# Performance work log

Hardware: AMD Instinct MI355X
Metric: run time of the kernel (lower is better)

## Reference

```python
import jax, jax.numpy as jnp
import numpy as np

TEMPERATURE = 8.0  # sqrt(d_k=64)
NEG_INF = -1.0e9   # matches masked_fill value in source


def setup_inputs() -> dict:
    key = jax.random.key(0)
    kq, kk, kv, km = jax.random.split(key, 4)
    B, H, T, C = 2, 16, 2048, 64
    q = jax.random.normal(kq, (B, H, T, C), dtype=jnp.float32)
    k = jax.random.normal(kk, (B, H, T, C), dtype=jnp.float32)
    v = jax.random.normal(kv, (B, H, T, C), dtype=jnp.float32)
    mask = jax.random.randint(km, (B, 1, T, T), 0, 2, dtype=jnp.int32)
    return {"q": q, "k": k, "v": v, "mask": mask}


def reference(q, k, v, mask):
    # attn = (q / temperature) @ k^T   -> [b, h, T, T]
    attn = jnp.einsum("bhqc,bhkc->bhqk", q / TEMPERATURE, k)
    attn = jnp.where(mask == 0, NEG_INF, attn)
    attn = jax.nn.softmax(attn, axis=-1)
    # dropout is identity in eval / deterministic reference
    output = jnp.einsum("bhqk,bhkc->bhqc", attn, v)
    return (output, attn)
```

## Files before the change

### kernel.cpp

```cpp
#include <hip/hip_runtime.h>
#include <stdint.h>
#include <stddef.h>

#define T_DIM 2048
#define C_DIM 64
#define SCALE_L2E 0.18033688011112042f
#define STG_P 40

typedef __bf16 bf16x8 __attribute__((ext_vector_type(8)));
typedef float f32x4 __attribute__((ext_vector_type(4)));
typedef unsigned int u32x4 __attribute__((ext_vector_type(4)));
typedef unsigned int u32x2 __attribute__((ext_vector_type(2)));
typedef int i32x4 __attribute__((ext_vector_type(4)));
typedef unsigned short u16t;

static __device__ __forceinline__ unsigned f2bf_bits(float f) {
  unsigned u = __builtin_bit_cast(unsigned, f);
  u += 0x7fffu + ((u >> 16) & 1u);
  return u >> 16;
}
static __device__ __forceinline__ bf16x8 asfrag(u32x4 u) {
  return __builtin_bit_cast(bf16x8, u);
}
static __device__ __forceinline__ bf16x8 pack8(f32x4 a, f32x4 b) {
  u32x4 u;
  u[0] = f2bf_bits(a[0]) | (f2bf_bits(a[1]) << 16);
  u[1] = f2bf_bits(a[2]) | (f2bf_bits(a[3]) << 16);
  u[2] = f2bf_bits(b[0]) | (f2bf_bits(b[1]) << 16);
  u[3] = f2bf_bits(b[2]) | (f2bf_bits(b[3]) << 16);
  return __builtin_bit_cast(bf16x8, u);
}
static __device__ __forceinline__ bf16x8 ld_cvt8(const float* p) {
  return pack8(*(const f32x4*)p, *(const f32x4*)(p + 4));
}
static __device__ __forceinline__ float bf_lo(unsigned u) {
  return __builtin_bit_cast(float, u << 16);
}
static __device__ __forceinline__ float bf_hi(unsigned u) {
  return __builtin_bit_cast(float, u & 0xffff0000u);
}

__global__ __launch_bounds__(256) void prep_kernel(
    const float* __restrict__ k, const float* __restrict__ v,
    const int* __restrict__ mask, u16t* __restrict__ kb,
    u16t* __restrict__ vt2, unsigned* __restrict__ mb) {
  if (blockIdx.x < 2048) {
    const size_t e0 = ((size_t)blockIdx.x * 256 + threadIdx.x) * 8;
    const float* src = k + e0;
    u32x4 u;
    f32x4 a = *(const f32x4*)src;
    f32x4 b = *(const f32x4*)(src + 4);
    u[0] = f2bf_bits(a[0]) | (f2bf_bits(a[1]) << 16);
    u[1] = f2bf_bits(a[2]) | (f2bf_bits(a[3]) << 16);
    u[2] = f2bf_bits(b[0]) | (f2bf_bits(b[1]) << 16);
    u[3] = f2bf_bits(b[2]) | (f2bf_bits(b[3]) << 16);
    *(u32x4*)(kb + e0) = u;
  } else if (blockIdx.x < 4096) {
    __shared__ float tile[32][66];
    const int t = threadIdx.x;
    const int tl = blockIdx.x - 2048;
    const int bh = tl >> 6;
    const int t32 = tl & 63;
    const float* src = v + ((size_t)bh * T_DIM + t32 * 32) * C_DIM;
#pragma unroll
    for (int u = 0; u < 2; ++u) {
      const int vec = t + u * 256;
      const int jj = vec >> 4;
      const int c4 = (vec & 15) * 4;
      const f32x4 x = *(const f32x4*)(src + jj * C_DIM + c4);
      tile[jj][c4] = x[0];
      tile[jj][c4 + 1] = x[1];
      tile[jj][c4 + 2] = x[2];
      tile[jj][c4 + 3] = x[3];
    }
    __syncthreads();
    const int c = t >> 2;
    const int j8 = (t & 3) * 8;
    u32x4 o;
#pragma unroll
    for (int i = 0; i < 4; ++i) {
      o[i] = f2bf_bits(tile[j8 + 2 * i][c]) |
             (f2bf_bits(tile[j8 + 2 * i + 1][c]) << 16);
    }
    *(u32x4*)(vt2 + ((size_t)bh * 64 + t32) * 2048 + (size_t)t * 8) = o;
  } else {
    const int gid = (blockIdx.x - 4096) * 256 + threadIdx.x;
    const int* src = mask + (size_t)gid * 32;
    unsigned bits = 0;
#pragma unroll
    for (int t = 0; t < 8; ++t) {
      i32x4 x = *(const i32x4*)(src + t * 4);
      bits |= (x[0] != 0 ? 1u : 0u) << (t * 4);
      bits |= (x[1] != 0 ? 1u : 0u) << (t * 4 + 1);
      bits |= (x[2] != 0 ? 1u : 0u) << (t * 4 + 2);
      bits |= (x[3] != 0 ? 1u : 0u) << (t * 4 + 3);
    }
    mb[gid] = bits;
  }
}

template <bool USE_PREP>
__global__ __launch_bounds__(256, 3) void attn_fwd(
    const float* __restrict__ qp, const float* __restrict__ kp,
    const float* __restrict__ vp, const int* __restrict__ maskp,
    const u16t* __restrict__ kbp, const u16t* __restrict__ vt2p,
    const unsigned* __restrict__ mbp, float* __restrict__ outp,
    float* __restrict__ attnp) {
  __shared__ float Of[4096];
  __shared__ u16t stg[4][2][16 * STG_P];
  __shared__ float rowsum[64];
  __shared__ float rls[16];

  const int tid = threadIdx.x;
  const int wave = tid >> 6;
  const int lane = tid & 63;
  const int quad = lane >> 4;
  const int l15 = lane & 15;

  const int h = blockIdx.x & 15;
  const int qb = (blockIdx.x >> 4) & 127;
  const int b = blockIdx.x >> 11;
  const int bh = b * 16 + h;
  const int q0 = qb << 4;

  const float* qrow = qp + ((size_t)bh * T_DIM + q0 + l15) * C_DIM + quad * 8;
  const bf16x8 qf0 = ld_cvt8(qrow);
  const bf16x8 qf1 = ld_cvt8(qrow + 32);

  const u16t* kbbase = kbp + (size_t)bh * T_DIM * C_DIM;
  const float* kfbase = kp + (size_t)bh * T_DIM * C_DIM;
  const float* vfbase = vp + (size_t)bh * T_DIM * C_DIM;
  const u16t* vtbase = vt2p + (size_t)bh * (C_DIM * T_DIM) +
                       (size_t)wave * 16 * 2048 + l15 * 32 + quad * 8;
  const unsigned* mrowb =
      mbp + ((size_t)b * T_DIM + q0 + l15) * (T_DIM / 32) + wave * 16;
  const int* mrow = maskp + ((size_t)b * T_DIM + q0 + l15) * T_DIM;

  f32x4 ao0 = {0.f, 0.f, 0.f, 0.f};
  f32x4 ao1 = {0.f, 0.f, 0.f, 0.f};
  f32x4 ao2 = {0.f, 0.f, 0.f, 0.f};
  f32x4 ao3 = {0.f, 0.f, 0.f, 0.f};
  u32x2 pA[16], pB[16];
  float ls0 = 0.f, ls1 = 0.f;

#pragma unroll
  for (int s = 0; s < 16; ++s) {
    const int j0 = wave * 512 + s * 32;

    bf16x8 kA0, kA1, kB0, kB1;
    u32x4 vb0, vb1, vb2, vb3;
    unsigned mq = 0;
    i32x4 mA, mB;
    if constexpr (USE_PREP) {
      const u16t* ka = kbbase + (size_t)(j0 + l15) * C_DIM + quad * 8;
      kA0 = asfrag(*(const u32x4*)(ka));
      kA1 = asfrag(*(const u32x4*)(ka + 32));
      kB0 = asfrag(*(const u32x4*)(ka + 16 * C_DIM));
      kB1 = asfrag(*(const u32x4*)(ka + 16 * C_DIM + 32));
      const u16t* tb = vtbase + (size_t)s * 2048;
      vb0 = *(const u32x4*)(tb);
      vb1 = *(const u32x4*)(tb + 512);
      vb2 = *(const u32x4*)(tb + 1024);
      vb3 = *(const u32x4*)(tb + 1536);
      mq = mrowb[s] >> (quad * 4);
    } else {
      const float* ka = kfbase + (size_t)(j0 + l15) * C_DIM + quad * 8;
      kA0 = ld_cvt8(ka);
      kA1 = ld_cvt8(ka + 32);
      kB0 = ld_cvt8(ka + 16 * C_DIM);
      kB1 = ld_cvt8(ka + 16 * C_DIM + 32);
      const float* g = vfbase + (size_t)(j0 + quad * 8) * C_DIM + l15;
      auto gather = [&](int c0) -> u32x4 {
        const float* p = g + c0;
        u32x4 r;
        r[0] = f2bf_bits(p[0]) | (f2bf_bits(p[C_DIM]) << 16);
        r[1] = f2bf_bits(p[2 * C_DIM]) | (f2bf_bits(p[3 * C_DIM]) << 16);
        r[2] = f2bf_bits(p[4 * C_DIM]) | (f2bf_bits(p[5 * C_DIM]) << 16);
        r[3] = f2bf_bits(p[6 * C_DIM]) | (f2bf_bits(p[7 * C_DIM]) << 16);
        return r;
      };
      vb0 = gather(0); vb1 = gather(16); vb2 = gather(32); vb3 = gather(48);
      mA = *(const i32x4*)(mrow + j0 + quad * 4);
      mB = *(const i32x4*)(mrow + j0 + 16 + quad * 4);
    }

    f32x4 sA = {0.f, 0.f, 0.f, 0.f};
    sA = __builtin_amdgcn_mfma_f32_16x16x32_bf16(kA0, qf0, sA, 0, 0, 0);
    sA = __builtin_amdgcn_mfma_f32_16x16x32_bf16(kA1, qf1, sA, 0, 0, 0);
    f32x4 sB = {0.f, 0.f, 0.f, 0.f};
    sB = __builtin_amdgcn_mfma_f32_16x16x32_bf16(kB0, qf0, sB, 0, 0, 0);
    sB = __builtin_amdgcn_mfma_f32_16x16x32_bf16(kB1, qf1, sB, 0, 0, 0);

    const float eA0 = __builtin_exp2f(sA[0] * SCALE_L2E);
    const float eA1 = __builtin_exp2f(sA[1] * SCALE_L2E);
    const float eA2 = __builtin_exp2f(sA[2] * SCALE_L2E);
    const float eA3 = __builtin_exp2f(sA[3] * SCALE_L2E);
    const float eB0 = __builtin_exp2f(sB[0] * SCALE_L2E);
    const float eB1 = __builtin_exp2f(sB[1] * SCALE_L2E);
    const float eB2 = __builtin_exp2f(sB[2] * SCALE_L2E);
    const float eB3 = __builtin_exp2f(sB[3] * SCALE_L2E);
    float a0, a1, a2, a3, b0, b1, b2, b3;
    if constexpr (USE_PREP) {
      a0 = (mq & 0x1u) ? eA0 : 0.f;
      a1 = (mq & 0x2u) ? eA1 : 0.f;
      a2 = (mq & 0x4u) ? eA2 : 0.f;
      a3 = (mq & 0x8u) ? eA3 : 0.f;
      b0 = (mq & 0x10000u) ? eB0 : 0.f;
      b1 = (mq & 0x20000u) ? eB1 : 0.f;
      b2 = (mq & 0x40000u) ? eB2 : 0.f;
      b3 = (mq & 0x80000u) ? eB3 : 0.f;
    } else {
      a0 = mA[0] ? eA0 : 0.f;
      a1 = mA[1] ? eA1 : 0.f;
      a2 = mA[2] ? eA2 : 0.f;
      a3 = mA[3] ? eA3 : 0.f;
      b0 = mB[0] ? eB0 : 0.f;
      b1 = mB[1] ? eB1 : 0.f;
      b2 = mB[2] ? eB2 : 0.f;
      b3 = mB[3] ? eB3 : 0.f;
    }

    u32x2 wA, wB;
    wA[0] = f2bf_bits(a0) | (f2bf_bits(a1) << 16);
    wA[1] = f2bf_bits(a2) | (f2bf_bits(a3) << 16);
    wB[0] = f2bf_bits(b0) | (f2bf_bits(b1) << 16);
    wB[1] = f2bf_bits(b2) | (f2bf_bits(b3) << 16);
    pA[s] = wA;
    pB[s] = wB;

    ls0 += (a0 + a1) + (a2 + a3);
    ls1 += (b0 + b1) + (b2 + b3);

    u16t* const sb = stg[wave][s & 1];
    *(u32x2*)&sb[l15 * STG_P + quad * 4] = wA;
    *(u32x2*)&sb[l15 * STG_P + quad * 4 + 16] = wB;
    const bf16x8 pa = asfrag(*(const u32x4*)&sb[l15 * STG_P + quad * 8]);
    ao0 = __builtin_amdgcn_mfma_f32_16x16x32_bf16(pa, asfrag(vb0), ao0, 0, 0, 0);
    ao1 = __builtin_amdgcn_mfma_f32_16x16x32_bf16(pa, asfrag(vb1), ao1, 0, 0, 0);
    ao2 = __builtin_amdgcn_mfma_f32_16x16x32_bf16(pa, asfrag(vb2), ao2, 0, 0, 0);
    ao3 = __builtin_amdgcn_mfma_f32_16x16x32_bf16(pa, asfrag(vb3), ao3, 0, 0, 0);
  }

  float lsum = ls0 + ls1;
  lsum += __shfl_xor(lsum, 16, 64);
  lsum += __shfl_xor(lsum, 32, 64);
  if (quad == 0) rowsum[wave * 16 + l15] = lsum;
  __syncthreads();
  if (tid < 16)
    rls[tid] = 1.0f / (rowsum[tid] + rowsum[16 + tid] + rowsum[32 + tid] +
                       rowsum[48 + tid]);
  __syncthreads();

  const int brow = lane >> 3;
  const int bcol = (lane & 7) * 4;
  const float rlLo = rls[brow];
  const float rlHi = rls[8 + brow];
  float* const arowLo =
      attnp + ((size_t)bh * T_DIM + q0 + brow) * T_DIM + bcol;
  float* const arowHi = arowLo + (size_t)8 * T_DIM;
#pragma unroll
  for (int s = 0; s < 16; ++s) {
    const int j0 = wave * 512 + s * 32;
    u16t* const sb = stg[wave][s & 1];
    *(u32x2*)&sb[l15 * STG_P + quad * 4] = pA[s];
    *(u32x2*)&sb[l15 * STG_P + quad * 4 + 16] = pB[s];
    const u32x2 dlo = *(const u32x2*)&sb[brow * STG_P + bcol];
    const u32x2 dhi = *(const u32x2*)&sb[(8 + brow) * STG_P + bcol];
    f32x4 olo, ohi;
    olo[0] = bf_lo(dlo[0]) * rlLo;
    olo[1] = bf_hi(dlo[0]) * rlLo;
    olo[2] = bf_lo(dlo[1]) * rlLo;
    olo[3] = bf_hi(dlo[1]) * rlLo;
    ohi[0] = bf_lo(dhi[0]) * rlHi;
    ohi[1] = bf_hi(dhi[0]) * rlHi;
    ohi[2] = bf_lo(dhi[1]) * rlHi;
    ohi[3] = bf_hi(dhi[1]) * rlHi;
    *(f32x4*)(arowLo + j0) = olo;
    *(f32x4*)(arowHi + j0) = ohi;
  }

#pragma unroll
  for (int r = 0; r < 4; ++r) {
    const int qq = quad * 4 + r;
    float* dst = Of + wave * 1024 + qq * 64 + l15;
    dst[0] = ao0[r];
    dst[16] = ao1[r];
    dst[32] = ao2[r];
    dst[48] = ao3[r];
  }
  __syncthreads();
  {
    const int tq = tid >> 4;
    const int c = (tid & 15) * 4;
    f32x4 os = *(const f32x4*)&Of[tq * 64 + c];
    os += *(const f32x4*)&Of[1024 + tq * 64 + c];
    os += *(const f32x4*)&Of[2048 + tq * 64 + c];
    os += *(const f32x4*)&Of[3072 + tq * 64 + c];
    os *= rls[tq];
    *(f32x4*)(outp + ((size_t)bh * T_DIM + q0 + tq) * C_DIM + c) = os;
  }
}

extern "C" void kernel_launch(void* const* d_in, const int* in_sizes, int n_in,
                              void* d_out, int out_size, void* d_ws, size_t ws_size,
                              hipStream_t stream) {
  const float* q = (const float*)d_in[0];
  const float* k = (const float*)d_in[1];
  const float* v = (const float*)d_in[2];
  const int* mask = (const int*)d_in[3];
  float* out = (float*)d_out;
  float* attn = out + (size_t)2 * 16 * T_DIM * C_DIM;

  const size_t n_elems = (size_t)2 * 16 * T_DIM * C_DIM;
  const size_t n_mwords = (size_t)2 * T_DIM * (T_DIM / 32);
  const size_t prep_bytes = 2 * n_elems * sizeof(u16t) + n_mwords * 4;
  if (ws_size >= prep_bytes) {
    u16t* kb = (u16t*)d_ws;
    u16t* vt2 = kb + n_elems;
    unsigned* mb = (unsigned*)(vt2 + n_elems);
    prep_kernel<<<5120, 256, 0, stream>>>(k, v, mask, kb, vt2, mb);
    attn_fwd<true><<<4096, 256, 0, stream>>>(q, k, v, mask, kb, vt2, mb, out, attn);
  } else {
    attn_fwd<false><<<4096, 256, 0, stream>>>(q, k, v, mask, nullptr, nullptr,
                                              nullptr, out, attn);
  }
}
```

Baseline: 768.5 us.

## Use hardware bf16 packing, MFMA row sums, XCD-aware block mapping, setprio

Replaces manual round-to-nearest bf16 bit packing with native __bf16 conversions, which can lower to packed convert instructions. Computes softmax row sums with an extra MFMA against a ones vector instead of scalar adds and shuffles. Remaps block indices so each XCD handles contiguous heads for better L2 locality. Raises the occupancy hint to 4 blocks per CU and adds s_setprio around MFMA groups. The ones-MFMA sums the bf16-rounded probabilities, so normalisation uses slightly different values than the fp32 sums it replaces, and the higher occupancy target may cause register spills.

```diff
diff --git a/kernel.cpp b/kernel.cpp
--- a/kernel.cpp
+++ b/kernel.cpp
@@ -8,6 +8,7 @@
 #define STG_P 40
 
 typedef __bf16 bf16x8 __attribute__((ext_vector_type(8)));
+typedef __bf16 bf16x2t __attribute__((ext_vector_type(2)));
 typedef float f32x4 __attribute__((ext_vector_type(4)));
 typedef unsigned int u32x4 __attribute__((ext_vector_type(4)));
 typedef unsigned int u32x2 __attribute__((ext_vector_type(2)));
@@ -19,15 +20,21 @@
   u += 0x7fffu + ((u >> 16) & 1u);
   return u >> 16;
 }
+static __device__ __forceinline__ unsigned pk2(float a, float b) {
+  bf16x2t t;
+  t[0] = (__bf16)a;
+  t[1] = (__bf16)b;
+  return __builtin_bit_cast(unsigned, t);
+}
 static __device__ __forceinline__ bf16x8 asfrag(u32x4 u) {
   return __builtin_bit_cast(bf16x8, u);
 }
 static __device__ __forceinline__ bf16x8 pack8(f32x4 a, f32x4 b) {
   u32x4 u;
-  u[0] = f2bf_bits(a[0]) | (f2bf_bits(a[1]) << 16);
-  u[1] = f2bf_bits(a[2]) | (f2bf_bits(a[3]) << 16);
-  u[2] = f2bf_bits(b[0]) | (f2bf_bits(b[1]) << 16);
-  u[3] = f2bf_bits(b[2]) | (f2bf_bits(b[3]) << 16);
+  u[0] = pk2(a[0], a[1]);
+  u[1] = pk2(a[2], a[3]);
+  u[2] = pk2(b[0], b[1]);
+  u[3] = pk2(b[2], b[3]);
   return __builtin_bit_cast(bf16x8, u);
 }
 static __device__ __forceinline__ bf16x8 ld_cvt8(const float* p) {
@@ -50,10 +57,10 @@
     u32x4 u;
     f32x4 a = *(const f32x4*)src;
     f32x4 b = *(const f32x4*)(src + 4);
-    u[0] = f2bf_bits(a[0]) | (f2bf_bits(a[1]) << 16);
-    u[1] = f2bf_bits(a[2]) | (f2bf_bits(a[3]) << 16);
-    u[2] = f2bf_bits(b[0]) | (f2bf_bits(b[1]) << 16);
-    u[3] = f2bf_bits(b[2]) | (f2bf_bits(b[3]) << 16);
+    u[0] = pk2(a[0], a[1]);
+    u[1] = pk2(a[2], a[3]);
+    u[2] = pk2(b[0], b[1]);
+    u[3] = pk2(b[2], b[3]);
     *(u32x4*)(kb + e0) = u;
   } else if (blockIdx.x < 4096) {
     __shared__ float tile[32][66];
@@ -79,8 +86,7 @@
     u32x4 o;
 #pragma unroll
     for (int i = 0; i < 4; ++i) {
-      o[i] = f2bf_bits(tile[j8 + 2 * i][c]) |
-             (f2bf_bits(tile[j8 + 2 * i + 1][c]) << 16);
+      o[i] = pk2(tile[j8 + 2 * i][c], tile[j8 + 2 * i + 1][c]);
     }
     *(u32x4*)(vt2 + ((size_t)bh * 64 + t32) * 2048 + (size_t)t * 8) = o;
   } else {
@@ -100,7 +106,7 @@
 }
 
 template <bool USE_PREP>
-__global__ __launch_bounds__(256, 3) void attn_fwd(
+__global__ __launch_bounds__(256, 4) void attn_fwd(
     const float* __restrict__ qp, const float* __restrict__ kp,
     const float* __restrict__ vp, const int* __restrict__ maskp,
     const u16t* __restrict__ kbp, const u16t* __restrict__ vt2p,
@@ -117,10 +123,11 @@
   const int quad = lane >> 4;
   const int l15 = lane & 15;
 
-  const int h = blockIdx.x & 15;
-  const int qb = (blockIdx.x >> 4) & 127;
-  const int b = blockIdx.x >> 11;
-  const int bh = b * 16 + h;
+  const int xcd = blockIdx.x & 7;
+  const int slot = blockIdx.x >> 3;
+  const int bh = xcd * 4 + (slot >> 7);
+  const int qb = slot & 127;
+  const int b = bh >> 4;
   const int q0 = qb << 4;
 
   const float* qrow = qp + ((size_t)bh * T_DIM + q0 + l15) * C_DIM + quad * 8;
@@ -136,12 +143,17 @@
       mbp + ((size_t)b * T_DIM + q0 + l15) * (T_DIM / 32) + wave * 16;
   const int* mrow = maskp + ((size_t)b * T_DIM + q0 + l15) * T_DIM;
 
+  u32x4 onesw;
+  onesw[0] = 0x3F803F80u; onesw[1] = 0x3F803F80u;
+  onesw[2] = 0x3F803F80u; onesw[3] = 0x3F803F80u;
+  const bf16x8 onesf = asfrag(onesw);
+
   f32x4 ao0 = {0.f, 0.f, 0.f, 0.f};
   f32x4 ao1 = {0.f, 0.f, 0.f, 0.f};
   f32x4 ao2 = {0.f, 0.f, 0.f, 0.f};
   f32x4 ao3 = {0.f, 0.f, 0.f, 0.f};
+  f32x4 aoS = {0.f, 0.f, 0.f, 0.f};
   u32x2 pA[16], pB[16];
-  float ls0 = 0.f, ls1 = 0.f;
 
 #pragma unroll
   for (int s = 0; s < 16; ++s) {
@@ -173,10 +185,10 @@
       auto gather = [&](int c0) -> u32x4 {
         const float* p = g + c0;
         u32x4 r;
-        r[0] = f2bf_bits(p[0]) | (f2bf_bits(p[C_DIM]) << 16);
-        r[1] = f2bf_bits(p[2 * C_DIM]) | (f2bf_bits(p[3 * C_DIM]) << 16);
-        r[2] = f2bf_bits(p[4 * C_DIM]) | (f2bf_bits(p[5 * C_DIM]) << 16);
-        r[3] = f2bf_bits(p[6 * C_DIM]) | (f2bf_bits(p[7 * C_DIM]) << 16);
+        r[0] = pk2(p[0], p[C_DIM]);
+        r[1] = pk2(p[2 * C_DIM], p[3 * C_DIM]);
+        r[2] = pk2(p[4 * C_DIM], p[5 * C_DIM]);
+        r[3] = pk2(p[6 * C_DIM], p[7 * C_DIM]);
         return r;
       };
       vb0 = gather(0); vb1 = gather(16); vb2 = gather(32); vb3 = gather(48);
@@ -184,12 +196,14 @@
       mB = *(const i32x4*)(mrow + j0 + 16 + quad * 4);
     }
 
+    __builtin_amdgcn_s_setprio(1);
     f32x4 sA = {0.f, 0.f, 0.f, 0.f};
     sA = __builtin_amdgcn_mfma_f32_16x16x32_bf16(kA0, qf0, sA, 0, 0, 0);
     sA = __builtin_amdgcn_mfma_f32_16x16x32_bf16(kA1, qf1, sA, 0, 0, 0);
     f32x4 sB = {0.f, 0.f, 0.f, 0.f};
     sB = __builtin_amdgcn_mfma_f32_16x16x32_bf16(kB0, qf0, sB, 0, 0, 0);
     sB = __builtin_amdgcn_mfma_f32_16x16x32_bf16(kB1, qf1, sB, 0, 0, 0);
+    __builtin_amdgcn_s_setprio(0);
 
     const float eA0 = __builtin_exp2f(sA[0] * SCALE_L2E);
     const float eA1 = __builtin_exp2f(sA[1] * SCALE_L2E);
@@ -221,30 +235,30 @@
     }
 
     u32x2 wA, wB;
-    wA[0] = f2bf_bits(a0) | (f2bf_bits(a1) << 16);
-    wA[1] = f2bf_bits(a2) | (f2bf_bits(a3) << 16);
-    wB[0] = f2bf_bits(b0) | (f2bf_bits(b1) << 16);
-    wB[1] = f2bf_bits(b2) | (f2bf_bits(b3) << 16);
+    wA[0] = pk2(a0, a1);
+    wA[1] = pk2(a2, a3);
+    wB[0] = pk2(b0, b1);
+    wB[1] = pk2(b2, b3);
     pA[s] = wA;
     pB[s] = wB;
-
-    ls0 += (a0 + a1) + (a2 + a3);
-    ls1 += (b0 + b1) + (b2 + b3);
 
     u16t* const sb = stg[wave][s & 1];
     *(u32x2*)&sb[l15 * STG_P + quad * 4] = wA;
     *(u32x2*)&sb[l15 * STG_P + quad * 4 + 16] = wB;
     const bf16x8 pa = asfrag(*(const u32x4*)&sb[l15 * STG_P + quad * 8]);
+    __builtin_amdgcn_s_setprio(1);
     ao0 = __builtin_amdgcn_mfma_f32_16x16x32_bf16(pa, asfrag(vb0), ao0, 0, 0, 0);
     ao1 = __builtin_amdgcn_mfma_f32_16x16x32_bf16(pa, asfrag(vb1), ao1, 0, 0, 0);
     ao2 = __builtin_amdgcn_mfma_f32_16x16x32_bf16(pa, asfrag(vb2), ao2, 0, 0, 0);
     ao3 = __builtin_amdgcn_mfma_f32_16x16x32_bf16(pa, asfrag(vb3), ao3, 0, 0, 0);
-  }
-
-  float lsum = ls0 + ls1;
-  lsum += __shfl_xor(lsum, 16, 64);
-  lsum += __shfl_xor(lsum, 32, 64);
-  if (quad == 0) rowsum[wave * 16 + l15] = lsum;
+    aoS = __builtin_amdgcn_mfma_f32_16x16x32_bf16(pa, onesf, aoS, 0, 0, 0);
+    __builtin_amdgcn_s_setprio(0);
+  }
+
+  if (l15 == 0) {
+#pragma unroll
+    for (int r = 0; r < 4; ++r) rowsum[wave * 16 + quad * 4 + r] = aoS[r];
+  }
   __syncthreads();
   if (tid < 16)
     rls[tid] = 1.0f / (rowsum[tid] + rowsum[16 + tid] + rowsum[32 + tid] +
```

Measured after the change: 739.0 us. 3.8% less time.
